# Optimization experiments

Measured on AMD Instinct MI355X. Metric: run time of the kernel, lower is better.

## Reference

```python
import jax, jax.numpy as jnp
import numpy as np

NUM_HEAD = 8


def setup_inputs() -> dict:
    key = jax.random.key(0)
    ks = jax.random.split(key, 4)
    B, nd, nh, nw, N, C = 1, 4, 4, 4, 512, 512
    x = jax.random.normal(ks[0], (B, nd, nh, nw, N, C), dtype=jnp.float32)
    w_qkv = jax.random.normal(ks[1], (C, 3 * C), dtype=jnp.float32) / np.sqrt(C).astype(np.float32)
    b_qkv = jnp.zeros((3 * C,), dtype=jnp.float32)
    w_proj = jax.random.normal(ks[2], (C, C), dtype=jnp.float32) / np.sqrt(C).astype(np.float32)
    b_proj = jnp.zeros((C,), dtype=jnp.float32)
    return {"x": x, "w_qkv": w_qkv, "b_qkv": b_qkv, "w_proj": w_proj, "b_proj": b_proj}


def reference(x, w_qkv, b_qkv, w_proj, b_proj):
    B, nd, nh, nw, N, C = x.shape
    hd = C // NUM_HEAD
    # QKV projection, split into q/k/v with per-head layout [B,nd,nh,nw,N,H,hd]
    qkv = (x @ w_qkv + b_qkv).reshape(B, nd, nh, nw, N, 3, NUM_HEAD, hd)
    q = qkv[..., 0, :, :]
    k = qkv[..., 1, :, :]
    v = qkv[..., 2, :, :]
    # Block-local attention. NOTE: original module defines self.scale but never
    # applies it in forward, so no 1/sqrt(hd) scaling here (faithful to source).
    attn = jnp.einsum('...qhd,...khd->...hqk', q, k)  # [B,nd,nh,nw,H,N,N]
    attn = jax.nn.softmax(attn, axis=-1)
    out = jnp.einsum('...hqk,...khd->...qhd', attn, v)  # [B,nd,nh,nw,N,H,hd]
    out = out.reshape(B, nd, nh, nw, N, C)
    return out @ w_proj + b_proj
```

## Files before the change

### kernel.cpp

```cpp
#include <hip/hip_runtime.h>
#include <hip/hip_bf16.h>

typedef _Float16 half8_t __attribute__((ext_vector_type(8)));
typedef _Float16 half4_t __attribute__((ext_vector_type(4)));
typedef _Float16 half2_t __attribute__((ext_vector_type(2)));
typedef float    f32x4   __attribute__((ext_vector_type(4)));
typedef float    f32x16  __attribute__((ext_vector_type(16)));

#define CDIM 512
#define NHEAD 8
#define HD 64
#define NTOK 512
#define NWIN 64
#define TC 1536

__device__ __forceinline__ float fexp2(float x) {
  float r;
  asm("v_exp_f32 %0, %1" : "=v"(r) : "v"(x));
  return r;
}

#define GLL16(g, l)                                                        \
  __builtin_amdgcn_global_load_lds((const __attribute__((address_space(1))) void*)(g), \
                                   (__attribute__((address_space(3))) void*)(l), 16, 0, 0)


__global__ __launch_bounds__(256) void cvt_x(const float* __restrict__ x,
                                             _Float16* __restrict__ x16, int n8) {
  int i = blockIdx.x * 256 + threadIdx.x;
  if (i < n8) {
    float4 v0 = *(const float4*)(x + (size_t)i * 8);
    float4 v1 = *(const float4*)(x + (size_t)i * 8 + 4);
    half8_t h = {(_Float16)v0.x, (_Float16)v0.y, (_Float16)v0.z, (_Float16)v0.w,
                 (_Float16)v1.x, (_Float16)v1.y, (_Float16)v1.z, (_Float16)v1.w};
    *(half8_t*)(x16 + (size_t)i * 8) = h;
  }
}

__global__ __launch_bounds__(256) void prep_weights(
    const float* __restrict__ wqkv, const float* __restrict__ wproj,
    _Float16* __restrict__ wqkvT, _Float16* __restrict__ wprojT) {
  __shared__ _Float16 T[64 * 65];
  int b = blockIdx.x;
  const float* src; _Float16* dst; int Cc, r0, c0;
  if (b < 192) {
    src = wqkv; dst = wqkvT; Cc = 1536;
    c0 = (b % 24) * 64; r0 = (b / 24) * 64;
  } else {
    b -= 192; src = wproj; dst = wprojT; Cc = 512;
    c0 = (b & 7) * 64; r0 = (b >> 3) * 64;
  }
  const int t = threadIdx.x;
#pragma unroll
  for (int i = 0; i < 16; ++i) {
    int idx = i * 256 + t, rr = idx >> 6, cc = idx & 63;
    T[rr * 65 + cc] = (_Float16)src[(size_t)(r0 + rr) * Cc + c0 + cc];
  }
  __syncthreads();
#pragma unroll
  for (int i = 0; i < 2; ++i) {
    int idx = i * 256 + t, ol = idx >> 3, c8 = idx & 7;
    half8_t vv;
#pragma unroll
    for (int e = 0; e < 8; ++e) vv[e] = T[(c8 * 8 + e) * 65 + ol];
    *(half8_t*)(dst + (size_t)(c0 + ol) * 512 + r0 + c8 * 8) = vv;
  }
}

__global__ __launch_bounds__(512, 2) void gemm1_qkv(
    const _Float16* __restrict__ x16,
    const _Float16* __restrict__ wT,
    const float* __restrict__ bias,
    _Float16* __restrict__ qkv) {
  __shared__ __align__(16) char ring[4 * 32768];
  char* ringB = ring;
  const int tid = threadIdx.x;
  const int l = tid & 63;
  const int wid = tid >> 6;
  const int wr = wid >> 2, wc = wid & 3;
  const int lr = l & 15, g = l >> 4;
  const int koff = ((g ^ ((lr >> 1) & 3)) << 4);
  const int m0 = blockIdx.x * 256;
  const int cb = blockIdx.y * 256;
  const int j = cb >> 9;

  const int srow4 = l >> 2;
  const int schk = (l & 3) ^ ((srow4 >> 1) & 3);
  const size_t aSrc = (size_t)(m0 + wid * 32 + srow4) * 1024 + ((size_t)schk << 4);
  const size_t bSrc = (size_t)(cb + wid * 32 + srow4) * 1024 + ((size_t)schk << 4);

#define ISSUE_G1(KS)                                                              \
  {                                                                               \
    char* sa = ringB + ((KS)&3) * 32768;                                          \
    char* sb = sa + 16384;                                                        \
    _Pragma("unroll") for (int i = 0; i < 2; ++i) {                               \
      GLL16((const char*)x16 + aSrc + (size_t)i * 16384 + (size_t)(KS)*64,        \
            sa + wid * 2048 + i * 1024);                                          \
      GLL16((const char*)wT + bSrc + (size_t)i * 16384 + (size_t)(KS)*64,         \
            sb + wid * 2048 + i * 1024);                                          \
    }                                                                             \
  }

  ISSUE_G1(0) ISSUE_G1(1) ISSUE_G1(2)

  f32x4 acc[8][4] = {};

#define GITER(KS, NW)                                                             \
  {                                                                               \
    asm volatile("s_waitcnt vmcnt(" NW ")" ::: "memory");                         \
    __builtin_amdgcn_sched_barrier(0);                                            \
    asm volatile("s_barrier" ::: "memory");                                       \
    if ((KS) + 3 < 16) ISSUE_G1((KS) + 3)                                         \
    char* sa = ringB + ((KS)&3) * 32768;                                          \
    char* sb = sa + 16384;                                                        \
    half8_t a[8], b[4];                                                           \
    _Pragma("unroll") for (int mt = 0; mt < 8; ++mt)                              \
        a[mt] = *(const half8_t*)(sa + (wr * 128 + mt * 16 + lr) * 64 + koff);    \
    _Pragma("unroll") for (int nt = 0; nt < 4; ++nt)                              \
        b[nt] = *(const half8_t*)(sb + (wc * 64 + nt * 16 + lr) * 64 + koff);     \
    __builtin_amdgcn_s_setprio(1);                                                \
    _Pragma("unroll") for (int mt = 0; mt < 8; ++mt)                              \
        _Pragma("unroll") for (int nt = 0; nt < 4; ++nt)                          \
            acc[mt][nt] =                                                         \
                __builtin_amdgcn_mfma_f32_16x16x32_f16(a[mt], b[nt], acc[mt][nt], 0, 0, 0); \
    __builtin_amdgcn_s_setprio(0);                                                \
  }

  GITER(0, "8")  GITER(1, "8")  GITER(2, "8")  GITER(3, "8")
  GITER(4, "8")  GITER(5, "8")  GITER(6, "8")  GITER(7, "8")
  GITER(8, "8")  GITER(9, "8")  GITER(10, "8") GITER(11, "8")
  GITER(12, "8") GITER(13, "8") GITER(14, "4") GITER(15, "0")

  if (j == 2) {
#pragma unroll
    for (int nt = 0; nt < 4; ++nt) {
      const int ch = cb + wc * 64 + nt * 16 + lr;
      const int h = (ch >> 6) & 7, d = ch & 63;
      const float bvs = bias[ch];
#pragma unroll
      for (int mt = 0; mt < 8; ++mt) {
        const int row = m0 + wr * 128 + mt * 16 + g * 4;
        const int wL = row >> 9, n = row & 511;
        _Float16* panel = qkv + ((size_t)(wL * 24 + 16 + h) << 15);
        const int kg = n >> 4, hh = (n >> 2) & 1, e4 = (n & 8) >> 1;
        half4_t pk = {(_Float16)(acc[mt][nt][0] + bvs), (_Float16)(acc[mt][nt][1] + bvs),
                      (_Float16)(acc[mt][nt][2] + bvs), (_Float16)(acc[mt][nt][3] + bvs)};
        *(half4_t*)(panel + ((size_t)(kg * 2 + hh) * 64 + d) * 8 + e4) = pk;
      }
    }
  } else {
    __syncthreads();
    const float scl = (j == 0) ? 1.44269504f : 1.0f;
    char* CB = ringB;
#pragma unroll
    for (int nt = 0; nt < 4; ++nt) {
      const int chl = wc * 64 + nt * 16 + lr;
      const float bvs = bias[cb + chl];
#pragma unroll
      for (int mt = 0; mt < 8; ++mt) {
#pragma unroll
        for (int r = 0; r < 4; ++r) {
          int nl = wr * 128 + mt * 16 + g * 4 + r;
          *(_Float16*)(CB + nl * 512 + ((chl * 2) ^ ((nl & 7) << 5))) =
              (_Float16)((acc[mt][nt][r] + bvs) * scl);
        }
      }
    }
    __syncthreads();
#pragma unroll
    for (int i = 0; i < 16; ++i) {
      int idx = i * 512 + tid, nl = idx >> 5, c8 = idx & 31;
      half8_t vv = *(const half8_t*)(CB + nl * 512 + ((c8 * 16) ^ ((nl & 7) << 5)));
      int chg = cb + c8 * 8;
      int h = (chg >> 6) & 7, d = chg & 63;
      int ng = m0 + nl, wL = ng >> 9, nn = ng & 511;
      _Float16* panel = qkv + ((size_t)(wL * 24 + j * 8 + h) << 15);
      *(half8_t*)(panel + (size_t)nn * 64 + d) = vv;
    }
  }
}

__global__ __launch_bounds__(512) void attn_win(_Float16* __restrict__ qkv) {
  __shared__ __align__(16) char ring[4 * 8192];
  char* ringB = ring;
  const int tid = threadIdx.x;
  const int l = tid & 63;
  const int wid = tid >> 6;
  const int q32 = l & 31;
  const int h2 = l >> 5;
  const int wh = blockIdx.x;
  const int qc = blockIdx.y;
  const int h = wh & 7;
  const int w = wh >> 3;
  _Float16* Qp = qkv + ((size_t)(w * 24 + h) << 15);
  const _Float16* Kp = qkv + ((size_t)(w * 24 + 8 + h) << 15);
  const _Float16* Vp = qkv + ((size_t)(w * 24 + 16 + h) << 15);
  const int qrow = qc * 256 + wid * 32 + q32;

  const size_t kSrc = (size_t)(l >> 3) * 128 + (size_t)((l & 7) ^ (l >> 3)) * 16;
  const int kof0 = ((0 * 2 + h2) ^ (q32 & 7)) << 4;
  const int kof1 = ((1 * 2 + h2) ^ (q32 & 7)) << 4;
  const int kof2 = ((2 * 2 + h2) ^ (q32 & 7)) << 4;
  const int kof3 = ((3 * 2 + h2) ^ (q32 & 7)) << 4;
  const int voff = 4096 + h2 * 1024 + q32 * 16;

#define ISSUE_SLOT(KT)                                                            \
  {                                                                               \
    char* sb = ringB + ((KT)&3) * 8192;                                           \
    if (wid < 4) {                                                                \
      GLL16((const char*)Kp + (size_t)(KT)*4096 + (size_t)wid * 1024 + kSrc,      \
            sb + wid * 1024);                                                     \
    } else {                                                                      \
      GLL16((const char*)Vp + (size_t)(KT)*4096 + (size_t)(wid - 4) * 1024 + l * 16, \
            sb + 4096 + (wid - 4) * 1024);                                        \
    }                                                                             \
  }

  half8_t qf[4];
#pragma unroll
  for (int j = 0; j < 4; ++j)
    qf[j] = *(const half8_t*)(Qp + (size_t)qrow * 64 + j * 16 + h2 * 8);
  asm volatile("s_waitcnt vmcnt(0)" ::: "memory");

  ISSUE_SLOT(0) ISSUE_SLOT(1) ISSUE_SLOT(2)

  f32x16 o0 = {}, o1 = {};
  float m_run = -1e30f, lsum = 0.f;

#define AITER(KT, NW)                                                             \
  {                                                                               \
    asm volatile("s_waitcnt vmcnt(" NW ")" ::: "memory");                         \
    __builtin_amdgcn_sched_barrier(0);                                            \
    asm volatile("s_barrier" ::: "memory");                                       \
    if ((KT) + 3 < 16) ISSUE_SLOT((KT) + 3)                                       \
    char* sl = ringB + ((KT)&3) * 8192;                                           \
    half8_t kf0 = *(const half8_t*)(sl + q32 * 128 + kof0);                       \
    half8_t kf1 = *(const half8_t*)(sl + q32 * 128 + kof1);                       \
    half8_t kf2 = *(const half8_t*)(sl + q32 * 128 + kof2);                       \
    half8_t kf3 = *(const half8_t*)(sl + q32 * 128 + kof3);                       \
    __builtin_amdgcn_s_setprio(1);                                                \
    f32x16 s = {};                                                                \
    s = __builtin_amdgcn_mfma_f32_32x32x16_f16(kf0, qf[0], s, 0, 0, 0);           \
    s = __builtin_amdgcn_mfma_f32_32x32x16_f16(kf1, qf[1], s, 0, 0, 0);           \
    s = __builtin_amdgcn_mfma_f32_32x32x16_f16(kf2, qf[2], s, 0, 0, 0);           \
    s = __builtin_amdgcn_mfma_f32_32x32x16_f16(kf3, qf[3], s, 0, 0, 0);           \
    __builtin_amdgcn_s_setprio(0);                                                \
    float ma = fmaxf(fmaxf(s[0], s[1]), s[2]);                                    \
    float mb = fmaxf(fmaxf(s[3], s[4]), s[5]);                                    \
    float mc = fmaxf(fmaxf(s[6], s[7]), s[8]);                                    \
    float md = fmaxf(fmaxf(s[9], s[10]), s[11]);                                  \
    float me = fmaxf(fmaxf(s[12], s[13]), s[14]);                                 \
    float mf_ = fmaxf(fmaxf(ma, mb), mc);                                         \
    float mg = fmaxf(fmaxf(md, me), s[15]);                                       \
    float tmax = fmaxf(mf_, mg);                                                  \
    tmax = fmaxf(tmax, __shfl_xor(tmax, 32));                                     \
    if (!__all(tmax <= m_run + 11.5f)) {                                          \
      float mNew = fmaxf(m_run, tmax);                                            \
      float sc = fexp2(m_run - mNew);                                             \
      lsum *= sc;                                                                 \
      _Pragma("unroll") for (int r = 0; r < 16; ++r) { o0[r] *= sc; o1[r] *= sc; }\
      m_run = mNew;                                                               \
    }                                                                             \
    half8_t pf0, pf1;                                                             \
    float tsum = 0.f;                                                             \
    _Pragma("unroll") for (int e = 0; e < 4; ++e) {                               \
      float a0 = fexp2(s[2 * e] - m_run), a1 = fexp2(s[2 * e + 1] - m_run);       \
      tsum += a0 + a1;                                                            \
      ((half2_t*)&pf0)[e] =                                                       \
          __builtin_bit_cast(half2_t, __builtin_amdgcn_cvt_pkrtz(a0, a1));        \
    }                                                                             \
    _Pragma("unroll") for (int e = 0; e < 4; ++e) {                               \
      float a0 = fexp2(s[8 + 2 * e] - m_run), a1 = fexp2(s[9 + 2 * e] - m_run);   \
      tsum += a0 + a1;                                                            \
      ((half2_t*)&pf1)[e] =                                                       \
          __builtin_bit_cast(half2_t, __builtin_amdgcn_cvt_pkrtz(a0, a1));        \
    }                                                                             \
    tsum += __shfl_xor(tsum, 32);                                                 \
    lsum += tsum;                                                                 \
    half8_t vf0 = *(const half8_t*)(sl + voff);                                   \
    half8_t vf1 = *(const half8_t*)(sl + voff + 512);                             \
    half8_t vf2 = *(const half8_t*)(sl + voff + 2048);                            \
    half8_t vf3 = *(const half8_t*)(sl + voff + 2560);                            \
    __builtin_amdgcn_s_setprio(1);                                                \
    o0 = __builtin_amdgcn_mfma_f32_32x32x16_f16(vf0, pf0, o0, 0, 0, 0);           \
    o1 = __builtin_amdgcn_mfma_f32_32x32x16_f16(vf1, pf0, o1, 0, 0, 0);           \
    o0 = __builtin_amdgcn_mfma_f32_32x32x16_f16(vf2, pf1, o0, 0, 0, 0);           \
    o1 = __builtin_amdgcn_mfma_f32_32x32x16_f16(vf3, pf1, o1, 0, 0, 0);           \
    __builtin_amdgcn_s_setprio(0);                                                \
  }

  AITER(0, "2")  AITER(1, "2")  AITER(2, "2")  AITER(3, "2")
  AITER(4, "2")  AITER(5, "2")  AITER(6, "2")  AITER(7, "2")
  AITER(8, "2")  AITER(9, "2")  AITER(10, "2") AITER(11, "2")
  AITER(12, "2") AITER(13, "2") AITER(14, "1") AITER(15, "0")

  const float inv = 1.0f / lsum;
#pragma unroll
  for (int rq = 0; rq < 4; ++rq) {
    half4_t v0, v1;
#pragma unroll
    for (int i = 0; i < 4; ++i) {
      v0[i] = (_Float16)(o0[rq * 4 + i] * inv);
      v1[i] = (_Float16)(o1[rq * 4 + i] * inv);
    }
    *(half4_t*)(Qp + (size_t)qrow * 64 + 8 * rq + 4 * h2) = v0;
    *(half4_t*)(Qp + (size_t)qrow * 64 + 32 + 8 * rq + 4 * h2) = v1;
  }
}

__global__ __launch_bounds__(256) void gemm2_proj(
    const _Float16* __restrict__ qkv,
    const _Float16* __restrict__ wpT,
    const float* __restrict__ bias,
    float* __restrict__ out) {
  const int tid = threadIdx.x, l = tid & 63;
  const int wid = tid >> 6, wr = wid >> 1, wc = wid & 1;
  const int lr = l & 15, lk8 = (l >> 4) * 8;
  const int m0 = blockIdx.x * 128, n0 = blockIdx.y * 128;
  size_t aBase[4];
#pragma unroll
  for (int mt = 0; mt < 4; ++mt) {
    int row = m0 + wr * 64 + mt * 16 + lr;
    int wL = row >> 9, n = row & 511;
    aBase[mt] = ((size_t)(wL * 24) << 15) + (size_t)n * 64 + lk8;
  }
  size_t bBase[4];
#pragma unroll
  for (int nt = 0; nt < 4; ++nt)
    bBase[nt] = (size_t)(n0 + wc * 64 + nt * 16 + lr) * 512 + lk8;

  half8_t a[4], b[4];
#pragma unroll
  for (int mt = 0; mt < 4; ++mt) a[mt] = *(const half8_t*)(qkv + aBase[mt]);
#pragma unroll
  for (int nt = 0; nt < 4; ++nt) b[nt] = *(const half8_t*)(wpT + bBase[nt]);

  f32x4 acc[4][4] = {};
#pragma unroll 2
  for (int ks = 0; ks < 16; ++ks) {
    half8_t an[4], bn[4];
    if (ks < 15) {
      const size_t aoff = (size_t)((ks + 1) >> 1) * 32768 + (size_t)((ks + 1) & 1) * 32;
#pragma unroll
      for (int mt = 0; mt < 4; ++mt) an[mt] = *(const half8_t*)(qkv + aBase[mt] + aoff);
#pragma unroll
      for (int nt = 0; nt < 4; ++nt) bn[nt] = *(const half8_t*)(wpT + bBase[nt] + (ks + 1) * 32);
    }
#pragma unroll
    for (int mt = 0; mt < 4; ++mt)
#pragma unroll
      for (int nt = 0; nt < 4; ++nt)
        acc[mt][nt] = __builtin_amdgcn_mfma_f32_16x16x32_f16(a[mt], b[nt], acc[mt][nt], 0, 0, 0);
#pragma unroll
    for (int i = 0; i < 4; ++i) { a[i] = an[i]; b[i] = bn[i]; }
  }
#pragma unroll
  for (int nt = 0; nt < 4; ++nt) {
    int col = n0 + wc * 64 + nt * 16 + lr;
    float bv = bias[col];
#pragma unroll
    for (int mt = 0; mt < 4; ++mt) {
      int row = m0 + wr * 64 + mt * 16 + ((l >> 4) << 2);
#pragma unroll
      for (int r = 0; r < 4; ++r)
        out[(size_t)(row + r) * 512 + col] = acc[mt][nt][r] + bv;
    }
  }
}

extern "C" void kernel_launch(void* const* d_in, const int* in_sizes, int n_in,
                              void* d_out, int out_size, void* d_ws, size_t ws_size,
                              hipStream_t stream) {
  const float* x = (const float*)d_in[0];
  const float* wqkv = (const float*)d_in[1];
  const float* bqkv = (const float*)d_in[2];
  const float* wproj = (const float*)d_in[3];
  const float* bproj = (const float*)d_in[4];
  float* out = (float*)d_out;

  _Float16* wqkvT = (_Float16*)d_ws;
  _Float16* wprojT = wqkvT + (size_t)TC * CDIM;
  _Float16* chunkws = wprojT + (size_t)CDIM * CDIM;
  const size_t fixed = ((size_t)TC * CDIM + (size_t)CDIM * CDIM) * sizeof(_Float16);
  const size_t perwin = ((size_t)NTOK * CDIM + (size_t)24 * 32768) * sizeof(_Float16);
  int nw = 64;
  while (nw > 1 && fixed + (size_t)nw * perwin > ws_size) nw >>= 1;

  prep_weights<<<dim3(256), 256, 0, stream>>>(wqkv, wproj, wqkvT, wprojT);
  for (int wbase = 0; wbase < NWIN; wbase += nw) {
    const float* xc = x + (size_t)wbase * NTOK * CDIM;
    float* oc = out + (size_t)wbase * NTOK * CDIM;
    _Float16* x16 = chunkws;
    _Float16* qkvws = chunkws + (size_t)nw * NTOK * CDIM;
    const int n8 = nw * NTOK * CDIM / 8;
    cvt_x<<<dim3((n8 + 255) / 256), 256, 0, stream>>>(xc, x16, n8);
    gemm1_qkv<<<dim3(nw * 2, 6), 512, 0, stream>>>(x16, wqkvT, bqkv, qkvws);
    attn_win<<<dim3(nw * 8, 2), 512, 0, stream>>>(qkvws);
    gemm2_proj<<<dim3(nw * 4, 4), 256, 0, stream>>>(qkvws, wprojT, bproj, oc);
  }
}
```

Before: 216.7 us.

## Shrink QKV GEMM tiles to 128x128 and pre-block x and Wqkv into 16x32 tiles

The QKV projection GEMM moves from 256x256 tiles with 512 threads and a 4-stage LDS ring to 128x128 tiles with 256 threads, a 3-stage ring and launch bounds allowing three blocks per CU. The fp16 copies of x and Wqkv^T are now written in a blocked layout, so each 16-row by 32-column k-slice is a contiguous 1 KB chunk. That lets every global-to-LDS load in a pipeline step read contiguous memory instead of striding across rows. The aim is better occupancy, more blocks to spread across CUs, and more coalesced loads. The cost is lower data reuse per tile, so more global and L2 traffic for the operands, plus a shallower prefetch pipeline.

```diff
diff --git a/kernel.cpp b/kernel.cpp
--- a/kernel.cpp
+++ b/kernel.cpp
@@ -27,13 +27,16 @@
 
 __global__ __launch_bounds__(256) void cvt_x(const float* __restrict__ x,
                                              _Float16* __restrict__ x16, int n8) {
-  int i = blockIdx.x * 256 + threadIdx.x;
-  if (i < n8) {
-    float4 v0 = *(const float4*)(x + (size_t)i * 8);
-    float4 v1 = *(const float4*)(x + (size_t)i * 8 + 4);
-    half8_t h = {(_Float16)v0.x, (_Float16)v0.y, (_Float16)v0.z, (_Float16)v0.w,
-                 (_Float16)v1.x, (_Float16)v1.y, (_Float16)v1.z, (_Float16)v1.w};
-    *(half8_t*)(x16 + (size_t)i * 8) = h;
+  int idx = blockIdx.x * 256 + threadIdx.x;
+  if (idx < n8) {
+    int row = (idx * 8) >> 9;
+    int k = (idx * 8) & 511;
+    const float4 v0 = *(const float4*)(x + (size_t)row * 512 + k);
+    const float4 v1 = *(const float4*)(x + (size_t)row * 512 + k + 4);
+    half8_t hv = {(_Float16)v0.x, (_Float16)v0.y, (_Float16)v0.z, (_Float16)v0.w,
+                  (_Float16)v1.x, (_Float16)v1.y, (_Float16)v1.z, (_Float16)v1.w};
+    *(half8_t*)(x16 + (size_t)(row >> 4) * 8192 + (size_t)(k >> 5) * 512 +
+                (row & 15) * 32 + ((k & 31) >> 3) * 8) = hv;
   }
 }
 
@@ -42,12 +45,12 @@
     _Float16* __restrict__ wqkvT, _Float16* __restrict__ wprojT) {
   __shared__ _Float16 T[64 * 65];
   int b = blockIdx.x;
-  const float* src; _Float16* dst; int Cc, r0, c0;
+  const float* src; _Float16* dst; int Cc, r0, c0; bool blocked;
   if (b < 192) {
-    src = wqkv; dst = wqkvT; Cc = 1536;
+    src = wqkv; dst = wqkvT; Cc = 1536; blocked = true;
     c0 = (b % 24) * 64; r0 = (b / 24) * 64;
   } else {
-    b -= 192; src = wproj; dst = wprojT; Cc = 512;
+    b -= 192; src = wproj; dst = wprojT; Cc = 512; blocked = false;
     c0 = (b & 7) * 64; r0 = (b >> 3) * 64;
   }
   const int t = threadIdx.x;
@@ -63,73 +66,79 @@
     half8_t vv;
 #pragma unroll
     for (int e = 0; e < 8; ++e) vv[e] = T[(c8 * 8 + e) * 65 + ol];
-    *(half8_t*)(dst + (size_t)(c0 + ol) * 512 + r0 + c8 * 8) = vv;
-  }
-}
-
-__global__ __launch_bounds__(512, 2) void gemm1_qkv(
+    int o = c0 + ol, k = r0 + c8 * 8;
+    if (blocked)
+      *(half8_t*)(dst + (size_t)(o >> 4) * 8192 + (size_t)(k >> 5) * 512 +
+                  (o & 15) * 32 + ((k & 31) >> 3) * 8) = vv;
+    else
+      *(half8_t*)(dst + (size_t)o * 512 + k) = vv;
+  }
+}
+
+__global__ __launch_bounds__(256, 3) void gemm1_qkv(
     const _Float16* __restrict__ x16,
     const _Float16* __restrict__ wT,
     const float* __restrict__ bias,
     _Float16* __restrict__ qkv) {
-  __shared__ __align__(16) char ring[4 * 32768];
+  __shared__ __align__(16) char ring[3 * 16384];
   char* ringB = ring;
   const int tid = threadIdx.x;
   const int l = tid & 63;
   const int wid = tid >> 6;
-  const int wr = wid >> 2, wc = wid & 3;
+  const int wr = wid >> 1, wc = wid & 1;
   const int lr = l & 15, g = l >> 4;
   const int koff = ((g ^ ((lr >> 1) & 3)) << 4);
-  const int m0 = blockIdx.x * 256;
-  const int cb = blockIdx.y * 256;
+  const int m0 = blockIdx.x * 128;
+  const int cb = blockIdx.y * 128;
   const int j = cb >> 9;
 
-  const int srow4 = l >> 2;
-  const int schk = (l & 3) ^ ((srow4 >> 1) & 3);
-  const size_t aSrc = (size_t)(m0 + wid * 32 + srow4) * 1024 + ((size_t)schk << 4);
-  const size_t bSrc = (size_t)(cb + wid * 32 + srow4) * 1024 + ((size_t)schk << 4);
+  const int r4 = l >> 2;
+  const int schk = (l & 3) ^ ((r4 >> 1) & 3);
+  const size_t laneT = (size_t)r4 * 64 + (size_t)schk * 16;
+  const size_t aTile = ((size_t)(blockIdx.x * 8 + wid * 2)) * 16384 + laneT;
+  const size_t bTile = ((size_t)(blockIdx.y * 8 + wid * 2)) * 16384 + laneT;
 
 #define ISSUE_G1(KS)                                                              \
   {                                                                               \
-    char* sa = ringB + ((KS)&3) * 32768;                                          \
-    char* sb = sa + 16384;                                                        \
+    char* sa = ringB + ((KS) % 3) * 16384;                                        \
+    char* sbB = sa + 8192;                                                        \
     _Pragma("unroll") for (int i = 0; i < 2; ++i) {                               \
-      GLL16((const char*)x16 + aSrc + (size_t)i * 16384 + (size_t)(KS)*64,        \
+      GLL16((const char*)x16 + aTile + (size_t)i * 16384 + (size_t)(KS)*1024,     \
             sa + wid * 2048 + i * 1024);                                          \
-      GLL16((const char*)wT + bSrc + (size_t)i * 16384 + (size_t)(KS)*64,         \
-            sb + wid * 2048 + i * 1024);                                          \
+      GLL16((const char*)wT + bTile + (size_t)i * 16384 + (size_t)(KS)*1024,      \
+            sbB + wid * 2048 + i * 1024);                                         \
     }                                                                             \
   }
 
-  ISSUE_G1(0) ISSUE_G1(1) ISSUE_G1(2)
-
-  f32x4 acc[8][4] = {};
+  ISSUE_G1(0) ISSUE_G1(1)
+
+  f32x4 acc[4][4] = {};
 
 #define GITER(KS, NW)                                                             \
   {                                                                               \
     asm volatile("s_waitcnt vmcnt(" NW ")" ::: "memory");                         \
     __builtin_amdgcn_sched_barrier(0);                                            \
     asm volatile("s_barrier" ::: "memory");                                       \
-    if ((KS) + 3 < 16) ISSUE_G1((KS) + 3)                                         \
-    char* sa = ringB + ((KS)&3) * 32768;                                          \
-    char* sb = sa + 16384;                                                        \
-    half8_t a[8], b[4];                                                           \
-    _Pragma("unroll") for (int mt = 0; mt < 8; ++mt)                              \
-        a[mt] = *(const half8_t*)(sa + (wr * 128 + mt * 16 + lr) * 64 + koff);    \
+    if ((KS) + 2 < 16) ISSUE_G1((KS) + 2)                                         \
+    char* sa = ringB + ((KS) % 3) * 16384;                                        \
+    char* sbB = sa + 8192;                                                        \
+    half8_t a[4], b[4];                                                           \
+    _Pragma("unroll") for (int mt = 0; mt < 4; ++mt)                              \
+        a[mt] = *(const half8_t*)(sa + (wr * 64 + mt * 16 + lr) * 64 + koff);     \
     _Pragma("unroll") for (int nt = 0; nt < 4; ++nt)                              \
-        b[nt] = *(const half8_t*)(sb + (wc * 64 + nt * 16 + lr) * 64 + koff);     \
+        b[nt] = *(const half8_t*)(sbB + (wc * 64 + nt * 16 + lr) * 64 + koff);    \
     __builtin_amdgcn_s_setprio(1);                                                \
-    _Pragma("unroll") for (int mt = 0; mt < 8; ++mt)                              \
+    _Pragma("unroll") for (int mt = 0; mt < 4; ++mt)                              \
         _Pragma("unroll") for (int nt = 0; nt < 4; ++nt)                          \
             acc[mt][nt] =                                                         \
                 __builtin_amdgcn_mfma_f32_16x16x32_f16(a[mt], b[nt], acc[mt][nt], 0, 0, 0); \
     __builtin_amdgcn_s_setprio(0);                                                \
   }
 
-  GITER(0, "8")  GITER(1, "8")  GITER(2, "8")  GITER(3, "8")
-  GITER(4, "8")  GITER(5, "8")  GITER(6, "8")  GITER(7, "8")
-  GITER(8, "8")  GITER(9, "8")  GITER(10, "8") GITER(11, "8")
-  GITER(12, "8") GITER(13, "8") GITER(14, "4") GITER(15, "0")
+  GITER(0, "4")  GITER(1, "4")  GITER(2, "4")  GITER(3, "4")
+  GITER(4, "4")  GITER(5, "4")  GITER(6, "4")  GITER(7, "4")
+  GITER(8, "4")  GITER(9, "4")  GITER(10, "4") GITER(11, "4")
+  GITER(12, "4") GITER(13, "4") GITER(14, "4") GITER(15, "0")
 
   if (j == 2) {
 #pragma unroll
@@ -138,8 +147,8 @@
       const int h = (ch >> 6) & 7, d = ch & 63;
       const float bvs = bias[ch];
 #pragma unroll
-      for (int mt = 0; mt < 8; ++mt) {
-        const int row = m0 + wr * 128 + mt * 16 + g * 4;
+      for (int mt = 0; mt < 4; ++mt) {
+        const int row = m0 + wr * 64 + mt * 16 + g * 4;
         const int wL = row >> 9, n = row & 511;
         _Float16* panel = qkv + ((size_t)(wL * 24 + 16 + h) << 15);
         const int kg = n >> 4, hh = (n >> 2) & 1, e4 = (n & 8) >> 1;
@@ -157,20 +166,20 @@
       const int chl = wc * 64 + nt * 16 + lr;
       const float bvs = bias[cb + chl];
 #pragma unroll
-      for (int mt = 0; mt < 8; ++mt) {
+      for (int mt = 0; mt < 4; ++mt) {
 #pragma unroll
         for (int r = 0; r < 4; ++r) {
-          int nl = wr * 128 + mt * 16 + g * 4 + r;
-          *(_Float16*)(CB + nl * 512 + ((chl * 2) ^ ((nl & 7) << 5))) =
+          int nl = wr * 64 + mt * 16 + g * 4 + r;
+          *(_Float16*)(CB + nl * 256 + ((chl * 2) ^ ((nl & 7) << 5))) =
               (_Float16)((acc[mt][nt][r] + bvs) * scl);
         }
       }
     }
     __syncthreads();
 #pragma unroll
-    for (int i = 0; i < 16; ++i) {
-      int idx = i * 512 + tid, nl = idx >> 5, c8 = idx & 31;
-      half8_t vv = *(const half8_t*)(CB + nl * 512 + ((c8 * 16) ^ ((nl & 7) << 5)));
+    for (int i = 0; i < 8; ++i) {
+      int idx = i * 256 + tid, nl = idx >> 4, c8 = idx & 15;
+      half8_t vv = *(const half8_t*)(CB + nl * 256 + ((c8 * 16) ^ ((nl & 7) << 5)));
       int chg = cb + c8 * 8;
       int h = (chg >> 6) & 7, d = chg & 63;
       int ng = m0 + nl, wL = ng >> 9, nn = ng & 511;
@@ -394,7 +403,7 @@
     _Float16* qkvws = chunkws + (size_t)nw * NTOK * CDIM;
     const int n8 = nw * NTOK * CDIM / 8;
     cvt_x<<<dim3((n8 + 255) / 256), 256, 0, stream>>>(xc, x16, n8);
-    gemm1_qkv<<<dim3(nw * 2, 6), 512, 0, stream>>>(x16, wqkvT, bqkv, qkvws);
+    gemm1_qkv<<<dim3(nw * 4, 12), 256, 0, stream>>>(x16, wqkvT, bqkv, qkvws);
     attn_win<<<dim3(nw * 8, 2), 512, 0, stream>>>(qkvws);
     gemm2_proj<<<dim3(nw * 4, 4), 256, 0, stream>>>(qkvws, wprojT, bproj, oc);
   }
```

Measured after the change: 222.3 us. +2.6%, slower.

## Write attention output in tiled layout and pipeline projection GEMM through LDS

Applied to the files above, without the earlier changes.

The attention kernel now writes its output into a separate buffer in a pre-tiled 16x32 block layout, and the projection weights are also stored in that blocked layout. gemm2_proj switches from direct per-lane global loads to a three-slot LDS ring filled with async global_load_lds, using swizzled reads and explicit waitcnt/barrier scheduling. The aim is coalesced, latency-hidden loads in the projection GEMM. In exchange it uses an extra workspace buffer, which may shrink the per-chunk window count when workspace is small.

```diff
diff --git a/kernel.cpp b/kernel.cpp
--- a/kernel.cpp
+++ b/kernel.cpp
@@ -42,12 +42,12 @@
     _Float16* __restrict__ wqkvT, _Float16* __restrict__ wprojT) {
   __shared__ _Float16 T[64 * 65];
   int b = blockIdx.x;
-  const float* src; _Float16* dst; int Cc, r0, c0;
+  const float* src; _Float16* dst; int Cc, r0, c0; bool blocked;
   if (b < 192) {
-    src = wqkv; dst = wqkvT; Cc = 1536;
+    src = wqkv; dst = wqkvT; Cc = 1536; blocked = false;
     c0 = (b % 24) * 64; r0 = (b / 24) * 64;
   } else {
-    b -= 192; src = wproj; dst = wprojT; Cc = 512;
+    b -= 192; src = wproj; dst = wprojT; Cc = 512; blocked = true;
     c0 = (b & 7) * 64; r0 = (b >> 3) * 64;
   }
   const int t = threadIdx.x;
@@ -63,7 +63,12 @@
     half8_t vv;
 #pragma unroll
     for (int e = 0; e < 8; ++e) vv[e] = T[(c8 * 8 + e) * 65 + ol];
-    *(half8_t*)(dst + (size_t)(c0 + ol) * 512 + r0 + c8 * 8) = vv;
+    int o = c0 + ol, k = r0 + c8 * 8;
+    if (blocked)
+      *(half8_t*)(dst + (size_t)(o >> 4) * 8192 + (size_t)(k >> 5) * 512 +
+                  (o & 15) * 32 + (k & 24)) = vv;
+    else
+      *(half8_t*)(dst + (size_t)o * 512 + k) = vv;
   }
 }
 
@@ -180,7 +185,8 @@
   }
 }
 
-__global__ __launch_bounds__(512) void attn_win(_Float16* __restrict__ qkv) {
+__global__ __launch_bounds__(512) void attn_win(const _Float16* __restrict__ qkv,
+                                                _Float16* __restrict__ obuf) {
   __shared__ __align__(16) char ring[4 * 8192];
   char* ringB = ring;
   const int tid = threadIdx.x;
@@ -192,7 +198,7 @@
   const int qc = blockIdx.y;
   const int h = wh & 7;
   const int w = wh >> 3;
-  _Float16* Qp = qkv + ((size_t)(w * 24 + h) << 15);
+  const _Float16* Qp = qkv + ((size_t)(w * 24 + h) << 15);
   const _Float16* Kp = qkv + ((size_t)(w * 24 + 8 + h) << 15);
   const _Float16* Vp = qkv + ((size_t)(w * 24 + 16 + h) << 15);
   const int qrow = qc * 256 + wid * 32 + q32;
@@ -295,6 +301,8 @@
   AITER(12, "2") AITER(13, "2") AITER(14, "1") AITER(15, "0")
 
   const float inv = 1.0f / lsum;
+  const size_t rbase = ((size_t)(w * 32 + qc * 16 + wid * 2 + (q32 >> 4))) * 8192 +
+                       (size_t)(q32 & 15) * 32 + 4 * h2;
 #pragma unroll
   for (int rq = 0; rq < 4; ++rq) {
     half4_t v0, v1;
@@ -303,64 +311,82 @@
       v0[i] = (_Float16)(o0[rq * 4 + i] * inv);
       v1[i] = (_Float16)(o1[rq * 4 + i] * inv);
     }
-    *(half4_t*)(Qp + (size_t)qrow * 64 + 8 * rq + 4 * h2) = v0;
-    *(half4_t*)(Qp + (size_t)qrow * 64 + 32 + 8 * rq + 4 * h2) = v1;
-  }
-}
-
-__global__ __launch_bounds__(256) void gemm2_proj(
-    const _Float16* __restrict__ qkv,
+    *(half4_t*)(obuf + rbase + (size_t)(h * 2 + 0) * 512 + 8 * rq) = v0;
+    *(half4_t*)(obuf + rbase + (size_t)(h * 2 + 1) * 512 + 8 * rq) = v1;
+  }
+}
+
+__global__ __launch_bounds__(256, 3) void gemm2_proj(
+    const _Float16* __restrict__ obuf,
     const _Float16* __restrict__ wpT,
     const float* __restrict__ bias,
     float* __restrict__ out) {
-  const int tid = threadIdx.x, l = tid & 63;
-  const int wid = tid >> 6, wr = wid >> 1, wc = wid & 1;
-  const int lr = l & 15, lk8 = (l >> 4) * 8;
-  const int m0 = blockIdx.x * 128, n0 = blockIdx.y * 128;
-  size_t aBase[4];
-#pragma unroll
-  for (int mt = 0; mt < 4; ++mt) {
-    int row = m0 + wr * 64 + mt * 16 + lr;
-    int wL = row >> 9, n = row & 511;
-    aBase[mt] = ((size_t)(wL * 24) << 15) + (size_t)n * 64 + lk8;
-  }
-  size_t bBase[4];
-#pragma unroll
-  for (int nt = 0; nt < 4; ++nt)
-    bBase[nt] = (size_t)(n0 + wc * 64 + nt * 16 + lr) * 512 + lk8;
-
-  half8_t a[4], b[4];
-#pragma unroll
-  for (int mt = 0; mt < 4; ++mt) a[mt] = *(const half8_t*)(qkv + aBase[mt]);
-#pragma unroll
-  for (int nt = 0; nt < 4; ++nt) b[nt] = *(const half8_t*)(wpT + bBase[nt]);
+  __shared__ __align__(16) char ring[3 * 16384];
+  char* ringB = ring;
+  const int tid = threadIdx.x;
+  const int l = tid & 63;
+  const int wid = tid >> 6;
+  const int wr = wid >> 1, wc = wid & 1;
+  const int lr = l & 15, g = l >> 4;
+  const int koff = ((g ^ ((lr >> 1) & 3)) << 4);
+  const int m0 = blockIdx.x * 128;
+  const int n0 = blockIdx.y * 128;
+
+  const int r4 = l >> 2;
+  const int schk = (l & 3) ^ ((r4 >> 1) & 3);
+  const size_t laneT = (size_t)r4 * 64 + (size_t)schk * 16;
+  const size_t aTile = ((size_t)(blockIdx.x * 8 + wid * 2)) * 16384 + laneT;
+  const size_t bTile = ((size_t)(blockIdx.y * 8 + wid * 2)) * 16384 + laneT;
+
+#define ISSUE_G2(KS)                                                              \
+  {                                                                               \
+    char* sa = ringB + ((KS) % 3) * 16384;                                        \
+    char* sbB = sa + 8192;                                                        \
+    _Pragma("unroll") for (int i = 0; i < 2; ++i) {                               \
+      GLL16((const char*)obuf + aTile + (size_t)i * 16384 + (size_t)(KS)*1024,    \
+            sa + wid * 2048 + i * 1024);                                          \
+      GLL16((const char*)wpT + bTile + (size_t)i * 16384 + (size_t)(KS)*1024,     \
+            sbB + wid * 2048 + i * 1024);                                         \
+    }                                                                             \
+  }
+
+  ISSUE_G2(0) ISSUE_G2(1)
 
   f32x4 acc[4][4] = {};
-#pragma unroll 2
-  for (int ks = 0; ks < 16; ++ks) {
-    half8_t an[4], bn[4];
-    if (ks < 15) {
-      const size_t aoff = (size_t)((ks + 1) >> 1) * 32768 + (size_t)((ks + 1) & 1) * 32;
-#pragma unroll
-      for (int mt = 0; mt < 4; ++mt) an[mt] = *(const half8_t*)(qkv + aBase[mt] + aoff);
-#pragma unroll
-      for (int nt = 0; nt < 4; ++nt) bn[nt] = *(const half8_t*)(wpT + bBase[nt] + (ks + 1) * 32);
-    }
-#pragma unroll
-    for (int mt = 0; mt < 4; ++mt)
-#pragma unroll
-      for (int nt = 0; nt < 4; ++nt)
-        acc[mt][nt] = __builtin_amdgcn_mfma_f32_16x16x32_f16(a[mt], b[nt], acc[mt][nt], 0, 0, 0);
-#pragma unroll
-    for (int i = 0; i < 4; ++i) { a[i] = an[i]; b[i] = bn[i]; }
-  }
+
+#define G2ITER(KS, NW)                                                            \
+  {                                                                               \
+    asm volatile("s_waitcnt vmcnt(" NW ")" ::: "memory");                         \
+    __builtin_amdgcn_sched_barrier(0);                                            \
+    asm volatile("s_barrier" ::: "memory");                                       \
+    if ((KS) + 2 < 16) ISSUE_G2((KS) + 2)                                         \
+    char* sa = ringB + ((KS) % 3) * 16384;                                        \
+    char* sbB = sa + 8192;                                                        \
+    half8_t a[4], b[4];                                                           \
+    _Pragma("unroll") for (int mt = 0; mt < 4; ++mt)                              \
+        a[mt] = *(const half8_t*)(sa + (wr * 64 + mt * 16 + lr) * 64 + koff);     \
+    _Pragma("unroll") for (int nt = 0; nt < 4; ++nt)                              \
+        b[nt] = *(const half8_t*)(sbB + (wc * 64 + nt * 16 + lr) * 64 + koff);    \
+    __builtin_amdgcn_s_setprio(1);                                                \
+    _Pragma("unroll") for (int mt = 0; mt < 4; ++mt)                              \
+        _Pragma("unroll") for (int nt = 0; nt < 4; ++nt)                          \
+            acc[mt][nt] =                                                         \
+                __builtin_amdgcn_mfma_f32_16x16x32_f16(a[mt], b[nt], acc[mt][nt], 0, 0, 0); \
+    __builtin_amdgcn_s_setprio(0);                                                \
+  }
+
+  G2ITER(0, "4")  G2ITER(1, "4")  G2ITER(2, "4")  G2ITER(3, "4")
+  G2ITER(4, "4")  G2ITER(5, "4")  G2ITER(6, "4")  G2ITER(7, "4")
+  G2ITER(8, "4")  G2ITER(9, "4")  G2ITER(10, "4") G2ITER(11, "4")
+  G2ITER(12, "4") G2ITER(13, "4") G2ITER(14, "4") G2ITER(15, "0")
+
 #pragma unroll
   for (int nt = 0; nt < 4; ++nt) {
     int col = n0 + wc * 64 + nt * 16 + lr;
-    float bv = bias[col];
+    float bv = bias[col & 511];
 #pragma unroll
     for (int mt = 0; mt < 4; ++mt) {
-      int row = m0 + wr * 64 + mt * 16 + ((l >> 4) << 2);
+      int row = m0 + wr * 64 + mt * 16 + g * 4;
 #pragma unroll
       for (int r = 0; r < 4; ++r)
         out[(size_t)(row + r) * 512 + col] = acc[mt][nt][r] + bv;
@@ -382,7 +408,8 @@
   _Float16* wprojT = wqkvT + (size_t)TC * CDIM;
   _Float16* chunkws = wprojT + (size_t)CDIM * CDIM;
   const size_t fixed = ((size_t)TC * CDIM + (size_t)CDIM * CDIM) * sizeof(_Float16);
-  const size_t perwin = ((size_t)NTOK * CDIM + (size_t)24 * 32768) * sizeof(_Float16);
+  const size_t perwin =
+      ((size_t)NTOK * CDIM + (size_t)24 * 32768 + (size_t)NTOK * CDIM) * sizeof(_Float16);
   int nw = 64;
   while (nw > 1 && fixed + (size_t)nw * perwin > ws_size) nw >>= 1;
 
@@ -392,10 +419,11 @@
     float* oc = out + (size_t)wbase * NTOK * CDIM;
     _Float16* x16 = chunkws;
     _Float16* qkvws = chunkws + (size_t)nw * NTOK * CDIM;
+    _Float16* obuf = qkvws + (size_t)nw * 24 * 32768;
     const int n8 = nw * NTOK * CDIM / 8;
     cvt_x<<<dim3((n8 + 255) / 256), 256, 0, stream>>>(xc, x16, n8);
     gemm1_qkv<<<dim3(nw * 2, 6), 512, 0, stream>>>(x16, wqkvT, bqkv, qkvws);
-    attn_win<<<dim3(nw * 8, 2), 512, 0, stream>>>(qkvws);
-    gemm2_proj<<<dim3(nw * 4, 4), 256, 0, stream>>>(qkvws, wprojT, bproj, oc);
-  }
-}
+    attn_win<<<dim3(nw * 8, 2), 512, 0, stream>>>(qkvws, obuf);
+    gemm2_proj<<<dim3(nw * 4, 4), 256, 0, stream>>>(obuf, wprojT, bproj, oc);
+  }
+}
```

Result: faster. 185.1 us, median of 2 (-14.6%).
